# Performance work log

Measured on AMD Instinct MI355X. Metric: run time of the kernel, lower is better.

## Reference

```python
import jax, jax.numpy as jnp
import numpy as np

N = 100000      # nodes
E = 1600000     # edges (before self-loops)
IN_C = 128
HID = 32
HEADS = 4
NEG_SLOPE = 0.2  # PyG GATConv default


def gat_layer(x, W, a_src, a_dst, b, src, dst, n, heads, out_c, concat):
    # x: [n, F_in], W: [F_in, heads*out_c]
    h = (x @ W).reshape(n, heads, out_c)                      # [n, H, C]
    as_n = (h * a_src).sum(-1)                                # [n, H]
    ad_n = (h * a_dst).sum(-1)                                # [n, H]
    e = jax.nn.leaky_relu(as_n[src] + ad_n[dst], NEG_SLOPE)   # [E, H]
    # softmax over incoming edges of each destination node
    m = jax.ops.segment_max(e, dst, num_segments=n)           # [n, H]
    ee = jnp.exp(e - m[dst])
    denom = jax.ops.segment_sum(ee, dst, num_segments=n)      # [n, H]
    alpha = ee / (denom[dst] + 1e-16)                         # [E, H]
    out = jax.ops.segment_sum(h[src] * alpha[:, :, None], dst, num_segments=n)  # [n, H, C]
    out = out.reshape(n, heads * out_c) if concat else out.mean(axis=1)
    return out + b


def setup_inputs() -> dict:
    key = jax.random.key(0)
    ks = jax.random.split(key, 12)
    x = jax.random.normal(ks[0], (N, IN_C), dtype=jnp.float32)
    edge_index = jax.random.randint(ks[1], (2, E), 0, N, dtype=jnp.int64)
    s = 0.1
    return {
        "x": x,
        "edge_index": edge_index,
        "w1": jax.random.normal(ks[2], (IN_C, HEADS * HID), dtype=jnp.float32) * s,
        "a1_src": jax.random.normal(ks[3], (HEADS, HID), dtype=jnp.float32) * s,
        "a1_dst": jax.random.normal(ks[4], (HEADS, HID), dtype=jnp.float32) * s,
        "b1": jnp.zeros((HEADS * HID,), dtype=jnp.float32),
        "w2": jax.random.normal(ks[5], (HEADS * HID, HID), dtype=jnp.float32) * s,
        "a2_src": jax.random.normal(ks[6], (1, HID), dtype=jnp.float32) * s,
        "a2_dst": jax.random.normal(ks[7], (1, HID), dtype=jnp.float32) * s,
        "b2": jnp.zeros((HID,), dtype=jnp.float32),
        "wl": jax.random.normal(ks[8], (HID, 1), dtype=jnp.float32) * s,
        "bl": jnp.zeros((1,), dtype=jnp.float32),
    }


def reference(x, edge_index, w1, a1_src, a1_dst, b1, w2, a2_src, a2_dst, b2, wl, bl):
    n = x.shape[0]
    loop = jnp.arange(n, dtype=edge_index.dtype)
    # PyG GATConv adds self-loops by default
    src = jnp.concatenate([edge_index[0], loop])
    dst = jnp.concatenate([edge_index[1], loop])
    h = jax.nn.elu(gat_layer(x, w1, a1_src, a1_dst, b1, src, dst, n, HEADS, HID, True))
    h = jax.nn.elu(gat_layer(h, w2, a2_src, a2_dst, b2, src, dst, n, 1, HID, False))
    return (h @ wl + bl).squeeze(-1)   # [n]
```

## Files before the change

### kernel.cpp

```cpp
#include <hip/hip_runtime.h>
#include <math.h>

__device__ __forceinline__ float leaky02(float v) { return v > 0.f ? v : 0.2f * v; }
__device__ __forceinline__ float eluf(float v) { return v > 0.f ? v : __expf(v) - 1.f; }
__device__ __forceinline__ float expc(float v) { return __expf(fminf(v, 60.f)); }
__device__ __forceinline__ unsigned short f2bf(float f) {
    unsigned int u = __float_as_uint(f);
    return (unsigned short)((u + 0x7FFFu + ((u >> 16) & 1u)) >> 16);
}
__device__ __forceinline__ float bflo(unsigned int u) { return __uint_as_float(u << 16); }
__device__ __forceinline__ float bfhi(unsigned int u) { return __uint_as_float(u & 0xFFFF0000u); }

__global__ __launch_bounds__(256) void k_init1(int* __restrict__ p, int n) {
    int t = blockIdx.x * 256 + threadIdx.x;
    if (t < n) p[t] = 1;
}

__global__ __launch_bounds__(256, 2) void k_gemm1(
    const float* __restrict__ x, const float* __restrict__ w1,
    const float* __restrict__ a1s, const float* __restrict__ a1d,
    unsigned short* __restrict__ h1b, float* __restrict__ as1, float* __restrict__ ad1, int N)
{
    __shared__ float xs[64 * 128];
    __shared__ float wsh[128 * 64];
    const int half = blockIdx.x & 1;
    const int tile = blockIdx.x >> 1;
    const int tid  = threadIdx.x;
    const int r_base = tile * 64;

    for (int i = tid; i < 2048; i += 256) {
        int k = i >> 4, c4 = i & 15;
        float4 v = *(const float4*)(w1 + k * 128 + half * 64 + c4 * 4);
        *(float4*)(wsh + k * 64 + c4 * 4) = v;
    }
    for (int i = tid; i < 2048; i += 256) {
        int r = i >> 5, k4 = i & 31;
        int rr = r_base + r; if (rr >= N) rr = N - 1;
        float4 v = *(const float4*)(x + (size_t)rr * 128 + k4 * 4);
        *(float4*)(xs + r * 128 + (k4 ^ (r & 7)) * 4) = v;
    }
    __syncthreads();

    const int c0 = (tid & 15) * 4;
    const int r0 = (tid >> 4) * 4;
    const int swz0 = ((r0 + 0) & 7) << 2;
    const int swz1 = ((r0 + 1) & 7) << 2;
    const int swz2 = ((r0 + 2) & 7) << 2;
    const int swz3 = ((r0 + 3) & 7) << 2;
    const float* xb0 = xs + (r0 + 0) * 128;
    const float* xb1 = xs + (r0 + 1) * 128;
    const float* xb2 = xs + (r0 + 2) * 128;
    const float* xb3 = xs + (r0 + 3) * 128;

    float4 acc0 = {0,0,0,0}, acc1 = {0,0,0,0}, acc2 = {0,0,0,0}, acc3 = {0,0,0,0};
#pragma unroll 4
    for (int k = 0; k < 128; ++k) {
        float4 wv = *(const float4*)(wsh + k * 64 + c0);
        float x0 = xb0[k ^ swz0];
        float x1 = xb1[k ^ swz1];
        float x2 = xb2[k ^ swz2];
        float x3 = xb3[k ^ swz3];
        acc0.x = fmaf(x0, wv.x, acc0.x); acc0.y = fmaf(x0, wv.y, acc0.y);
        acc0.z = fmaf(x0, wv.z, acc0.z); acc0.w = fmaf(x0, wv.w, acc0.w);
        acc1.x = fmaf(x1, wv.x, acc1.x); acc1.y = fmaf(x1, wv.y, acc1.y);
        acc1.z = fmaf(x1, wv.z, acc1.z); acc1.w = fmaf(x1, wv.w, acc1.w);
        acc2.x = fmaf(x2, wv.x, acc2.x); acc2.y = fmaf(x2, wv.y, acc2.y);
        acc2.z = fmaf(x2, wv.z, acc2.z); acc2.w = fmaf(x2, wv.w, acc2.w);
        acc3.x = fmaf(x3, wv.x, acc3.x); acc3.y = fmaf(x3, wv.y, acc3.y);
        acc3.z = fmaf(x3, wv.z, acc3.z); acc3.w = fmaf(x3, wv.w, acc3.w);
    }

    const int cg = half * 64 + c0;
    const float4 avs = *(const float4*)(a1s + cg);
    const float4 avd = *(const float4*)(a1d + cg);
    const int head = half * 2 + ((tid & 15) >> 3);
    float4 accs[4] = {acc0, acc1, acc2, acc3};
#pragma unroll
    for (int i = 0; i < 4; ++i) {
        int r = r_base + r0 + i;
        float4 a = accs[i];
        float ps = a.x * avs.x + a.y * avs.y + a.z * avs.z + a.w * avs.w;
        float pd = a.x * avd.x + a.y * avd.y + a.z * avd.z + a.w * avd.w;
        ps += __shfl_xor(ps, 1); pd += __shfl_xor(pd, 1);
        ps += __shfl_xor(ps, 2); pd += __shfl_xor(pd, 2);
        ps += __shfl_xor(ps, 4); pd += __shfl_xor(pd, 4);
        if (r < N) {
            ushort4 hb;
            hb.x = f2bf(a.x); hb.y = f2bf(a.y); hb.z = f2bf(a.z); hb.w = f2bf(a.w);
            *(ushort4*)(h1b + (size_t)r * 128 + cg) = hb;
            if ((tid & 7) == 0) {
                as1[(size_t)r * 4 + head] = ps;
                ad1[(size_t)r * 4 + head] = pd;
            }
        }
    }
}

__global__ __launch_bounds__(256) void k_hist(const int* __restrict__ ei, int* __restrict__ counts,
                                              int E) {
    int t = blockIdx.x * 256 + threadIdx.x;
    if (t >= E) return;
    atomicAdd(&counts[ei[E + t]], 1);
}

__global__ __launch_bounds__(256) void k_bsum(const int* __restrict__ counts,
                                              int* __restrict__ bsum, int N) {
    int t = threadIdx.x;
    int base = blockIdx.x * 1024 + t * 4;
    int s = 0;
    if (base + 3 < N) { int4 v = *(const int4*)(counts + base); s = v.x + v.y + v.z + v.w; }
    else { for (int j = 0; j < 4; ++j) if (base + j < N) s += counts[base + j]; }
#pragma unroll
    for (int off = 1; off < 64; off <<= 1) s += __shfl_xor(s, off);
    __shared__ int wt[4];
    if ((t & 63) == 0) wt[t >> 6] = s;
    __syncthreads();
    if (t == 0) bsum[blockIdx.x] = wt[0] + wt[1] + wt[2] + wt[3];
}

__global__ __launch_bounds__(1024) void k_scansums(const int* __restrict__ bsum,
                                                   int* __restrict__ boff,
                                                   int* __restrict__ rowp_last, int NB) {
    __shared__ int ps[1024];
    int t = threadIdx.x;
    int v = (t < NB) ? bsum[t] : 0;
    ps[t] = v;
    __syncthreads();
    for (int off = 1; off < 1024; off <<= 1) {
        int u = (t >= off) ? ps[t - off] : 0;
        __syncthreads();
        ps[t] += u;
        __syncthreads();
    }
    if (t < NB) boff[t] = ps[t] - v;
    if (t == NB - 1) *rowp_last = ps[t];
}

__global__ __launch_bounds__(256) void k_scatter(const int* __restrict__ counts,
                                                 const int* __restrict__ boff,
                                                 int* __restrict__ rowp, int* __restrict__ pos, int N) {
    int t = threadIdx.x;
    int lane = t & 63, wv = t >> 6;
    int base = blockIdx.x * 1024 + t * 4;
    int c0 = 0, c1 = 0, c2 = 0, c3 = 0;
    if (base + 3 < N) { int4 v = *(const int4*)(counts + base); c0 = v.x; c1 = v.y; c2 = v.z; c3 = v.w; }
    else {
        if (base     < N) c0 = counts[base];
        if (base + 1 < N) c1 = counts[base + 1];
        if (base + 2 < N) c2 = counts[base + 2];
        if (base + 3 < N) c3 = counts[base + 3];
    }
    int ts = c0 + c1 + c2 + c3;
    int inc = ts;
#pragma unroll
    for (int off = 1; off < 64; off <<= 1) { int u = __shfl_up(inc, off); if (lane >= off) inc += u; }
    int excl = inc - ts;
    __shared__ int wt[4];
    if (lane == 63) wt[wv] = inc;
    __syncthreads();
    int woff = 0;
    for (int i = 0; i < wv; ++i) woff += wt[i];
    int p = boff[blockIdx.x] + woff + excl;
    if (base     < N) { rowp[base]     = p; pos[base]     = p; p += c0; }
    if (base + 1 < N) { rowp[base + 1] = p; pos[base + 1] = p; p += c1; }
    if (base + 2 < N) { rowp[base + 2] = p; pos[base + 2] = p; p += c2; }
    if (base + 3 < N) { rowp[base + 3] = p; pos[base + 3] = p; p += c3; }
}

__global__ __launch_bounds__(256) void k_fill(
    const int* __restrict__ ei, int* __restrict__ pos,
    int* __restrict__ col, int E, int Et)
{
    int t = blockIdx.x * 256 + threadIdx.x;
    if (t >= Et) return;
    int s, dd;
    if (t < E) { s = ei[t]; dd = ei[E + t]; } else { s = dd = t - E; }
    int p = atomicAdd(&pos[dd], 1);
    col[p] = s;
}

__global__ __launch_bounds__(256) void k_agg1(
    const int* __restrict__ rowp, const int* __restrict__ col,
    const float* __restrict__ as1, const float* __restrict__ ad1,
    const unsigned short* __restrict__ h1b,
    const float* __restrict__ b1, float* __restrict__ out1, int N)
{
    const int lane = threadIdx.x & 63;
    const int wid  = (blockIdx.x * 256 + threadIdx.x) >> 6;
    const int nw   = (gridDim.x * 256) >> 6;
    const int q    = lane >> 4;
    const int cl8  = lane & 15;
    const int hch  = cl8 >> 2;
    for (int n = wid; n < N; n += nw) {
        const int start = rowp[n], end = rowp[n + 1];
        const float4 ad4 = *(const float4*)(ad1 + (size_t)n * 4);
        float4 ds = {0.f, 0.f, 0.f, 0.f};
        for (int j = start + lane; j < end; j += 64) {
            int s = col[j];
            float4 a4 = *(const float4*)(as1 + (size_t)s * 4);
            ds.x += expc(leaky02(a4.x + ad4.x));
            ds.y += expc(leaky02(a4.y + ad4.y));
            ds.z += expc(leaky02(a4.z + ad4.z));
            ds.w += expc(leaky02(a4.w + ad4.w));
        }
#pragma unroll
        for (int sft = 1; sft < 64; sft <<= 1) {
            ds.x += __shfl_xor(ds.x, sft);
            ds.y += __shfl_xor(ds.y, sft);
            ds.z += __shfl_xor(ds.z, sft);
            ds.w += __shfl_xor(ds.w, sft);
        }
        const float dh  = (hch == 0) ? ds.x : (hch == 1) ? ds.y : (hch == 2) ? ds.z : ds.w;
        const float adh = (hch == 0) ? ad4.x : (hch == 1) ? ad4.y : (hch == 2) ? ad4.z : ad4.w;
        const float rdh = 1.f / (dh + 1e-16f);
        float acc[8] = {0.f,0.f,0.f,0.f,0.f,0.f,0.f,0.f};
        for (int j = start + q; j < end; j += 4) {
            int s = col[j];
            float asv = as1[(size_t)s * 4 + hch];
            float alpha = expc(leaky02(asv + adh)) * rdh;
            uint4 hv = *(const uint4*)(h1b + (size_t)s * 128 + cl8 * 8);
            acc[0] = fmaf(alpha, bflo(hv.x), acc[0]);
            acc[1] = fmaf(alpha, bfhi(hv.x), acc[1]);
            acc[2] = fmaf(alpha, bflo(hv.y), acc[2]);
            acc[3] = fmaf(alpha, bfhi(hv.y), acc[3]);
            acc[4] = fmaf(alpha, bflo(hv.z), acc[4]);
            acc[5] = fmaf(alpha, bfhi(hv.z), acc[5]);
            acc[6] = fmaf(alpha, bflo(hv.w), acc[6]);
            acc[7] = fmaf(alpha, bfhi(hv.w), acc[7]);
        }
#pragma unroll
        for (int i = 0; i < 8; ++i) {
            acc[i] += __shfl_xor(acc[i], 16);
            acc[i] += __shfl_xor(acc[i], 32);
        }
        if (q == 0) {
            float4 bv0 = *(const float4*)(b1 + cl8 * 8);
            float4 bv1 = *(const float4*)(b1 + cl8 * 8 + 4);
            float4 o0, o1;
            o0.x = eluf(acc[0] + bv0.x);
            o0.y = eluf(acc[1] + bv0.y);
            o0.z = eluf(acc[2] + bv0.z);
            o0.w = eluf(acc[3] + bv0.w);
            o1.x = eluf(acc[4] + bv1.x);
            o1.y = eluf(acc[5] + bv1.y);
            o1.z = eluf(acc[6] + bv1.z);
            o1.w = eluf(acc[7] + bv1.w);
            *(float4*)(out1 + (size_t)n * 128 + cl8 * 8)     = o0;
            *(float4*)(out1 + (size_t)n * 128 + cl8 * 8 + 4) = o1;
        }
    }
}

__global__ __launch_bounds__(256, 2) void k_gemm2(
    const float* __restrict__ out1, const float* __restrict__ w2,
    const float* __restrict__ a2s, const float* __restrict__ a2d,
    float* __restrict__ z2, float* __restrict__ as2, float* __restrict__ ad2, int N)
{
    __shared__ float xs[128 * 128];
    __shared__ float wsh[128 * 32];
    const int tid = threadIdx.x;
    const int r_base = blockIdx.x * 128;

    for (int i = tid; i < 1024; i += 256) {
        int k = i >> 3, c4 = i & 7;
        float4 v = *(const float4*)(w2 + k * 32 + c4 * 4);
        *(float4*)(wsh + k * 32 + c4 * 4) = v;
    }
    for (int i = tid; i < 4096; i += 256) {
        int r = i >> 5, k4 = i & 31;
        int rr = r_base + r; if (rr >= N) rr = N - 1;
        float4 v = *(const float4*)(out1 + (size_t)rr * 128 + k4 * 4);
        *(float4*)(xs + r * 128 + (k4 ^ (r & 7)) * 4) = v;
    }
    __syncthreads();

    const int c0 = (tid & 7) * 4;
    const int r0 = (tid >> 3) * 4;
    const int swz0 = ((r0 + 0) & 7) << 2;
    const int swz1 = ((r0 + 1) & 7) << 2;
    const int swz2 = ((r0 + 2) & 7) << 2;
    const int swz3 = ((r0 + 3) & 7) << 2;
    const float* xb0 = xs + (r0 + 0) * 128;
    const float* xb1 = xs + (r0 + 1) * 128;
    const float* xb2 = xs + (r0 + 2) * 128;
    const float* xb3 = xs + (r0 + 3) * 128;

    float4 acc0 = {0,0,0,0}, acc1 = {0,0,0,0}, acc2 = {0,0,0,0}, acc3 = {0,0,0,0};
#pragma unroll 4
    for (int k = 0; k < 128; ++k) {
        float4 wv = *(const float4*)(wsh + k * 32 + c0);
        float x0 = xb0[k ^ swz0];
        float x1 = xb1[k ^ swz1];
        float x2 = xb2[k ^ swz2];
        float x3 = xb3[k ^ swz3];
        acc0.x = fmaf(x0, wv.x, acc0.x); acc0.y = fmaf(x0, wv.y, acc0.y);
        acc0.z = fmaf(x0, wv.z, acc0.z); acc0.w = fmaf(x0, wv.w, acc0.w);
        acc1.x = fmaf(x1, wv.x, acc1.x); acc1.y = fmaf(x1, wv.y, acc1.y);
        acc1.z = fmaf(x1, wv.z, acc1.z); acc1.w = fmaf(x1, wv.w, acc1.w);
        acc2.x = fmaf(x2, wv.x, acc2.x); acc2.y = fmaf(x2, wv.y, acc2.y);
        acc2.z = fmaf(x2, wv.z, acc2.z); acc2.w = fmaf(x2, wv.w, acc2.w);
        acc3.x = fmaf(x3, wv.x, acc3.x); acc3.y = fmaf(x3, wv.y, acc3.y);
        acc3.z = fmaf(x3, wv.z, acc3.z); acc3.w = fmaf(x3, wv.w, acc3.w);
    }

    const float4 avs = *(const float4*)(a2s + c0);
    const float4 avd = *(const float4*)(a2d + c0);
    float4 accs[4] = {acc0, acc1, acc2, acc3};
#pragma unroll
    for (int i = 0; i < 4; ++i) {
        int r = r_base + r0 + i;
        float4 a = accs[i];
        float ps = a.x * avs.x + a.y * avs.y + a.z * avs.z + a.w * avs.w;
        float pd = a.x * avd.x + a.y * avd.y + a.z * avd.z + a.w * avd.w;
        ps += __shfl_xor(ps, 1); pd += __shfl_xor(pd, 1);
        ps += __shfl_xor(ps, 2); pd += __shfl_xor(pd, 2);
        ps += __shfl_xor(ps, 4); pd += __shfl_xor(pd, 4);
        if (r < N) {
            *(float4*)(z2 + (size_t)r * 32 + c0) = a;
            if ((tid & 7) == 0) { as2[r] = ps; ad2[r] = pd; }
        }
    }
}

__global__ __launch_bounds__(256) void k_agg2(
    const int* __restrict__ rowp, const int* __restrict__ col,
    const float* __restrict__ as2, const float* __restrict__ ad2,
    const float* __restrict__ z2, const float* __restrict__ b2,
    const float* __restrict__ wl, const float* __restrict__ bl,
    float* __restrict__ out, int N)
{
    const int lane = threadIdx.x & 63;
    const int wid  = (blockIdx.x * 256 + threadIdx.x) >> 6;
    const int nw   = (gridDim.x * 256) >> 6;
    const int q  = lane >> 4;
    const int cl = lane & 15;
    for (int n = wid; n < N; n += nw) {
        const int start = rowp[n], end = rowp[n + 1];
        const float adn = ad2[n];
        float d = 0.f;
        for (int j = start + lane; j < end; j += 64) {
            int s = col[j];
            d += expc(leaky02(as2[s] + adn));
        }
#pragma unroll
        for (int sft = 1; sft < 64; sft <<= 1) d += __shfl_xor(d, sft);
        const float rd = 1.f / (d + 1e-16f);
        float2 acc = {0.f, 0.f};
        for (int j = start + q; j < end; j += 4) {
            int s = col[j];
            float alpha = expc(leaky02(as2[s] + adn)) * rd;
            float2 zv = *(const float2*)(z2 + (size_t)s * 32 + cl * 2);
            acc.x = fmaf(alpha, zv.x, acc.x);
            acc.y = fmaf(alpha, zv.y, acc.y);
        }
        acc.x += __shfl_xor(acc.x, 16); acc.y += __shfl_xor(acc.y, 16);
        acc.x += __shfl_xor(acc.x, 32); acc.y += __shfl_xor(acc.y, 32);
        float h0 = eluf(acc.x + b2[cl * 2]);
        float h1v = eluf(acc.y + b2[cl * 2 + 1]);
        float p = h0 * wl[cl * 2] + h1v * wl[cl * 2 + 1];
#pragma unroll
        for (int sft = 1; sft < 16; sft <<= 1) p += __shfl_xor(p, sft);
        if (lane == 0) out[n] = p + bl[0];
    }
}

extern "C" void kernel_launch(void* const* d_in, const int* in_sizes, int n_in,
                              void* d_out, int out_size, void* d_ws, size_t ws_size,
                              hipStream_t stream) {
    const float* x   = (const float*)d_in[0];
    const int*   ei  = (const int*)d_in[1];
    const float* w1  = (const float*)d_in[2];
    const float* a1s = (const float*)d_in[3];
    const float* a1d = (const float*)d_in[4];
    const float* b1  = (const float*)d_in[5];
    const float* w2  = (const float*)d_in[6];
    const float* a2s = (const float*)d_in[7];
    const float* a2d = (const float*)d_in[8];
    const float* b2  = (const float*)d_in[9];
    const float* wl  = (const float*)d_in[10];
    const float* bl  = (const float*)d_in[11];
    float* out = (float*)d_out;

    const int N  = in_sizes[0] / 128;
    const int E  = in_sizes[1] / 2;
    const int Et = E + N;
    const int NB = (N + 1023) / 1024;

    float* ws   = (float*)d_ws;
    unsigned short* h1b = (unsigned short*)ws;
    float* out1 = ws   + (size_t)N * 64;
    float* as1  = out1 + (size_t)N * 128;
    float* ad1  = as1  + (size_t)N * 4;
    float* z2   = ad1  + (size_t)N * 4;
    float* as2  = z2   + (size_t)N * 32;
    float* ad2  = as2  + N;
    int* counts = (int*)(ad2 + N);
    int* rowp   = counts + N;
    int* col    = rowp + (N + 1);
    int* pos    = col + Et;
    int* bsum   = pos + N;
    int* boff   = bsum + NB;

    k_init1<<<(N + 255) / 256, 256, 0, stream>>>(counts, N);
    k_gemm1<<<2 * ((N + 63) / 64), 256, 0, stream>>>(x, w1, a1s, a1d, h1b, as1, ad1, N);
    k_hist<<<(E + 255) / 256, 256, 0, stream>>>(ei, counts, E);
    k_bsum<<<NB, 256, 0, stream>>>(counts, bsum, N);
    k_scansums<<<1, 1024, 0, stream>>>(bsum, boff, rowp + N, NB);
    k_scatter<<<NB, 256, 0, stream>>>(counts, boff, rowp, pos, N);
    k_fill<<<(Et + 255) / 256, 256, 0, stream>>>(ei, pos, col, E, Et);
    k_agg1<<<4096, 256, 0, stream>>>(rowp, col, as1, ad1, h1b, b1, out1, N);
    k_gemm2<<<(N + 127) / 128, 256, 0, stream>>>(out1, w2, a2s, a2d, z2, as2, ad2, N);
    k_agg2<<<4096, 256, 0, stream>>>(rowp, col, as2, ad2, z2, b2, wl, bl, out, N);
}
```

Measured before the change: 575.8 us.

## Build CSR via two-level bucket sort with shared-memory atomics

The direct per-destination atomic fill into col is replaced by a two-pass scheme. First, edges are bucketed into groups of 128 destination nodes using a global atomic per bucket, and (src,dst) pairs are written to a staging buffer. Then each bucket is sorted into col with shared-memory atomic counters. This aims to cut the scattered global atomics and random writes of the old fill, at the cost of an extra pass over the edges, a larger staging buffer, and heavy contention on the roughly 782 bucket counters. k_binit launches a single 1024-thread block, so it only handles N up to 131072.

```diff
diff --git a/kernel.cpp b/kernel.cpp
--- a/kernel.cpp
+++ b/kernel.cpp
@@ -138,7 +138,7 @@
 
 __global__ __launch_bounds__(256) void k_scatter(const int* __restrict__ counts,
                                                  const int* __restrict__ boff,
-                                                 int* __restrict__ rowp, int* __restrict__ pos, int N) {
+                                                 int* __restrict__ rowp, int N) {
     int t = threadIdx.x;
     int lane = t & 63, wv = t >> 6;
     int base = blockIdx.x * 1024 + t * 4;
@@ -161,22 +161,51 @@
     int woff = 0;
     for (int i = 0; i < wv; ++i) woff += wt[i];
     int p = boff[blockIdx.x] + woff + excl;
-    if (base     < N) { rowp[base]     = p; pos[base]     = p; p += c0; }
-    if (base + 1 < N) { rowp[base + 1] = p; pos[base + 1] = p; p += c1; }
-    if (base + 2 < N) { rowp[base + 2] = p; pos[base + 2] = p; p += c2; }
-    if (base + 3 < N) { rowp[base + 3] = p; pos[base + 3] = p; p += c3; }
-}
-
-__global__ __launch_bounds__(256) void k_fill(
-    const int* __restrict__ ei, int* __restrict__ pos,
-    int* __restrict__ col, int E, int Et)
+    if (base     < N) { rowp[base]     = p; p += c0; }
+    if (base + 1 < N) { rowp[base + 1] = p; p += c1; }
+    if (base + 2 < N) { rowp[base + 2] = p; p += c2; }
+    if (base + 3 < N) { rowp[base + 3] = p; p += c3; }
+}
+
+__global__ __launch_bounds__(1024) void k_binit(const int* __restrict__ rowp,
+                                                int* __restrict__ bq, int NBk) {
+    int t = threadIdx.x;
+    if (t < NBk) bq[t] = rowp[t * 128];
+}
+
+__global__ __launch_bounds__(256) void k_bucket(
+    const int* __restrict__ ei, int* __restrict__ bq,
+    int2* __restrict__ ebuf, int E, int Et)
 {
     int t = blockIdx.x * 256 + threadIdx.x;
     if (t >= Et) return;
     int s, dd;
     if (t < E) { s = ei[t]; dd = ei[E + t]; } else { s = dd = t - E; }
-    int p = atomicAdd(&pos[dd], 1);
-    col[p] = s;
+    int p = atomicAdd(&bq[dd >> 7], 1);
+    ebuf[p] = make_int2(s, dd);
+}
+
+__global__ __launch_bounds__(256) void k_csort(
+    const int* __restrict__ rowp, const int2* __restrict__ ebuf,
+    int* __restrict__ col, int N)
+{
+    __shared__ int cnt[128];
+    const int b = blockIdx.x;
+    const int nb0 = b * 128;
+    const int tid = threadIdx.x;
+    int nb1 = nb0 + 128; if (nb1 > N) nb1 = N;
+    if (tid < 128) {
+        int node = nb0 + tid;
+        cnt[tid] = (node < N) ? rowp[node] : 0;
+    }
+    __syncthreads();
+    const int j0 = rowp[nb0];
+    const int j1 = rowp[nb1];
+    for (int j = j0 + tid; j < j1; j += 256) {
+        int2 e = ebuf[j];
+        int p = atomicAdd(&cnt[e.y - nb0], 1);
+        col[p] = e.x;
+    }
 }
 
 __global__ __launch_bounds__(256) void k_agg1(
@@ -381,10 +410,11 @@
     const float* bl  = (const float*)d_in[11];
     float* out = (float*)d_out;
 
-    const int N  = in_sizes[0] / 128;
-    const int E  = in_sizes[1] / 2;
-    const int Et = E + N;
-    const int NB = (N + 1023) / 1024;
+    const int N   = in_sizes[0] / 128;
+    const int E   = in_sizes[1] / 2;
+    const int Et  = E + N;
+    const int NB  = (N + 1023) / 1024;
+    const int NBk = (N + 127) / 128;
 
     float* ws   = (float*)d_ws;
     unsigned short* h1b = (unsigned short*)ws;
@@ -397,17 +427,22 @@
     int* counts = (int*)(ad2 + N);
     int* rowp   = counts + N;
     int* col    = rowp + (N + 1);
-    int* pos    = col + Et;
-    int* bsum   = pos + N;
+    int* bsum   = col + Et;
     int* boff   = bsum + NB;
+    int* bq     = boff + NB;
+    uintptr_t ebase = (uintptr_t)(bq + NBk);
+    ebase = (ebase + 7) & ~(uintptr_t)7;
+    int2* ebuf  = (int2*)ebase;
 
     k_init1<<<(N + 255) / 256, 256, 0, stream>>>(counts, N);
     k_gemm1<<<2 * ((N + 63) / 64), 256, 0, stream>>>(x, w1, a1s, a1d, h1b, as1, ad1, N);
     k_hist<<<(E + 255) / 256, 256, 0, stream>>>(ei, counts, E);
     k_bsum<<<NB, 256, 0, stream>>>(counts, bsum, N);
     k_scansums<<<1, 1024, 0, stream>>>(bsum, boff, rowp + N, NB);
-    k_scatter<<<NB, 256, 0, stream>>>(counts, boff, rowp, pos, N);
-    k_fill<<<(Et + 255) / 256, 256, 0, stream>>>(ei, pos, col, E, Et);
+    k_scatter<<<NB, 256, 0, stream>>>(counts, boff, rowp, N);
+    k_binit<<<1, 1024, 0, stream>>>(rowp, bq, NBk);
+    k_bucket<<<(Et + 255) / 256, 256, 0, stream>>>(ei, bq, ebuf, E, Et);
+    k_csort<<<NBk, 256, 0, stream>>>(rowp, ebuf, col, N);
     k_agg1<<<4096, 256, 0, stream>>>(rowp, col, as1, ad1, h1b, b1, out1, N);
     k_gemm2<<<(N + 127) / 128, 256, 0, stream>>>(out1, w2, a2s, a2d, z2, as2, ad2, N);
     k_agg2<<<4096, 256, 0, stream>>>(rowp, col, as2, ad2, z2, b2, wl, bl, out, N);
```

Result: slower. 896.5 us (+55.7%).
